# Kernel optimization log

Measured on AMD Instinct MI355X. Metric: run time of the kernel, lower is better.

## Reference

```python
import jax, jax.numpy as jnp
import numpy as np

B, Q, LE, D, P, A = 8, 32, 128, 512, 32, 128


def setup_inputs() -> dict:
    key = jax.random.key(0)
    ks = jax.random.split(key, 8)
    exp_tokens = jax.random.normal(ks[0], (B, Q, LE, D), dtype=jnp.float32)
    exp_mask = jax.random.randint(ks[1], (B, Q, LE), 0, 2, dtype=jnp.int32)
    s_j = jax.random.normal(ks[2], (B, P, D), dtype=jnp.float32)
    req_mask = jax.random.randint(ks[3], (B, P), 0, 2, dtype=jnp.int32)
    sc = 1.0 / np.sqrt(D)
    Ws_w = jax.random.normal(ks[4], (A, D), dtype=jnp.float32) * sc
    Ws_b = jax.random.normal(ks[5], (A,), dtype=jnp.float32) * 0.01
    U_w = jax.random.normal(ks[6], (A, D), dtype=jnp.float32) * sc
    v_w = jax.random.normal(ks[7], (1, A), dtype=jnp.float32) * (1.0 / np.sqrt(A))
    return {"exp_tokens": exp_tokens, "exp_mask": exp_mask, "s_j": s_j,
            "req_mask": req_mask, "Ws_w": Ws_w, "Ws_b": Ws_b, "U_w": U_w, "v_w": v_w}


def reference(exp_tokens, exp_mask, s_j, req_mask, Ws_w, Ws_b, U_w, v_w):
    # ws: (B,P,A); uh: (B,Q,Le,A)
    ws = jnp.einsum('bpd,ad->bpa', s_j, Ws_w) + Ws_b
    uh = jnp.einsum('bqtd,ad->bqta', exp_tokens, U_w)
    # broadcast add -> (B,Q,P,Le,A), tanh, project with v -> (B,Q,P,Le)
    scored = jnp.tanh(uh[:, :, None, :, :] + ws[:, None, :, None, :])
    e = jnp.einsum('bqpta,a->bqpt', scored, v_w[0])
    tok_mask = exp_mask[:, :, None, :]  # (B,Q,1,Le) broadcast over P
    e = jnp.where(tok_mask == 0, jnp.float32(-1e9), e)
    # joint softmax over Q*Le per (b,p)
    e_t = jnp.transpose(e, (0, 2, 1, 3)).reshape(e.shape[0], e.shape[2], -1)
    a = jax.nn.softmax(e_t, axis=-1).reshape(e.shape[0], e.shape[2], e.shape[1], e.shape[3])
    a = jnp.transpose(a, (0, 2, 1, 3))  # (B,Q,P,Le)
    s_rlk = jnp.einsum('bqpt,bqtd->bqpd', a, exp_tokens)
    rmask = req_mask[:, None, :, None].astype(s_rlk.dtype)
    return s_rlk * rmask
```

## Files before the change

kernel.cpp:

```cpp
#include <hip/hip_runtime.h>
#include <hip/hip_bf16.h>

#define B_  8
#define Q_  32
#define LE_ 128
#define D_  512
#define P_  32
#define A_  128

typedef __attribute__((ext_vector_type(8))) short short8_t;
typedef __attribute__((ext_vector_type(4))) float floatx4_t;

__device__ __forceinline__ short f2bf(float x) {
    unsigned u = __float_as_uint(x);
    unsigned r = (u + 0x7fffu + ((u >> 16) & 1u)) >> 16;
    return (short)r;
}

__global__ __launch_bounds__(128) void ws_kernel(
    const float* __restrict__ s_j, const float* __restrict__ Ws_w,
    const float* __restrict__ Ws_b, float* __restrict__ ws) {
    __shared__ float s_row[D_];
    int bp = blockIdx.x;
    const float* src = s_j + (size_t)bp * D_;
    for (int i = threadIdx.x; i < D_; i += 128) s_row[i] = src[i];
    __syncthreads();
    int a = threadIdx.x;
    const float4* w4 = (const float4*)(Ws_w + (size_t)a * D_);
    const float4* s4 = (const float4*)s_row;
    float acc = 0.0f;
#pragma unroll 8
    for (int i = 0; i < D_ / 4; ++i) {
        float4 w = w4[i];
        float4 s = s4[i];
        acc += w.x * s.x + w.y * s.y + w.z * s.z + w.w * s.w;
    }
    ws[bp * A_ + a] = __expf(2.0f * (acc + Ws_b[a]));
}

#define TM_ 64
#define TBK_ 64
#define LDSP_ 72

__global__ __launch_bounds__(256, 2) void uh_mfma_kernel(
    const float* __restrict__ X, const float* __restrict__ W,
    float* __restrict__ uh) {
    __shared__ short As[TM_ * LDSP_];
    __shared__ short Bs[A_ * LDSP_];
    int mblk = blockIdx.x * TM_;
    int tid = threadIdx.x;
    int wave = tid >> 6, lane = tid & 63;
    int qd = lane >> 4, lr = lane & 15;
    int mh = wave >> 1, nh = wave & 1;

    floatx4_t acc[2][4];
#pragma unroll
    for (int i = 0; i < 2; ++i)
#pragma unroll
        for (int j = 0; j < 4; ++j) acc[i][j] = (floatx4_t){0.f, 0.f, 0.f, 0.f};

    int ra = tid >> 2, qa = tid & 3;
    int rb = tid >> 1, hb = tid & 1;

    for (int kt = 0; kt < D_ / TBK_; ++kt) {
        int k0 = kt * TBK_;
        __syncthreads();
        {
            const float4* src = (const float4*)(X + (size_t)(mblk + ra) * D_ + k0 + qa * 16);
            short* dst = As + ra * LDSP_ + qa * 16;
#pragma unroll
            for (int j = 0; j < 2; ++j) {
                float4 v0 = src[j * 2 + 0];
                float4 v1 = src[j * 2 + 1];
                short8_t s;
                s[0] = f2bf(v0.x); s[1] = f2bf(v0.y); s[2] = f2bf(v0.z); s[3] = f2bf(v0.w);
                s[4] = f2bf(v1.x); s[5] = f2bf(v1.y); s[6] = f2bf(v1.z); s[7] = f2bf(v1.w);
                *(short8_t*)(dst + j * 8) = s;
            }
        }
        {
            const float4* src = (const float4*)(W + (size_t)rb * D_ + k0 + hb * 32);
            short* dst = Bs + rb * LDSP_ + hb * 32;
#pragma unroll
            for (int j = 0; j < 4; ++j) {
                float4 v0 = src[j * 2 + 0];
                float4 v1 = src[j * 2 + 1];
                short8_t s;
                s[0] = f2bf(v0.x); s[1] = f2bf(v0.y); s[2] = f2bf(v0.z); s[3] = f2bf(v0.w);
                s[4] = f2bf(v1.x); s[5] = f2bf(v1.y); s[6] = f2bf(v1.z); s[7] = f2bf(v1.w);
                *(short8_t*)(dst + j * 8) = s;
            }
        }
        __syncthreads();
#pragma unroll
        for (int ks = 0; ks < 2; ++ks) {
            short8_t af[2], bf[4];
#pragma unroll
            for (int i = 0; i < 2; ++i)
                af[i] = *(const short8_t*)(As + (mh * 32 + i * 16 + lr) * LDSP_ + ks * 32 + qd * 8);
#pragma unroll
            for (int j = 0; j < 4; ++j)
                bf[j] = *(const short8_t*)(Bs + (nh * 64 + j * 16 + lr) * LDSP_ + ks * 32 + qd * 8);
#pragma unroll
            for (int i = 0; i < 2; ++i)
#pragma unroll
                for (int j = 0; j < 4; ++j)
                    acc[i][j] = __builtin_amdgcn_mfma_f32_16x16x32_bf16(af[i], bf[j], acc[i][j], 0, 0, 0);
        }
    }
#pragma unroll
    for (int i = 0; i < 2; ++i) {
#pragma unroll
        for (int j = 0; j < 4; ++j) {
            int mg = mblk + mh * 32 + i * 16 + qd * 4;
            int ng = nh * 64 + j * 16 + lr;
            float* dst = uh + (size_t)mg * A_ + ng;
#pragma unroll
            for (int r = 0; r < 4; ++r)
                dst[(size_t)r * A_] = __expf(2.0f * acc[i][j][r]);
        }
    }
}

__global__ __launch_bounds__(256) void score_kernel(
    const float* __restrict__ EU, const float* __restrict__ EW,
    const float* __restrict__ v_w, const int* __restrict__ exp_mask,
    float* __restrict__ e) {
    __shared__ float eu_t[32][132];
    __shared__ float ew_t[32][128];
    __shared__ float n2v[128];
    int blk = blockIdx.x;
    int bq = blk >> 2, tc = blk & 3;
    int b = bq >> 5;
    int t0 = tc * 32;
    int tid = threadIdx.x;

#pragma unroll
    for (int i = 0; i < 4; ++i) {
        int f = tid + i * 256;
        int t = f >> 5, a4 = f & 31;
        float4 v = *(const float4*)(EU + (size_t)(bq * LE_ + t0 + t) * A_ + a4 * 4);
        *(float4*)&eu_t[t][a4 * 4] = v;
    }
#pragma unroll
    for (int i = 0; i < 4; ++i) {
        int f = tid + i * 256;
        int p = f >> 5, a4 = f & 31;
        *(float4*)&ew_t[p][a4 * 4] =
            *(const float4*)(EW + (size_t)(b * P_ + p) * A_ + a4 * 4);
    }
    if (tid < 32) {
        float4 v = *(const float4*)(v_w + tid * 4);
        v.x *= -2.0f; v.y *= -2.0f; v.z *= -2.0f; v.w *= -2.0f;
        *(float4*)&n2v[tid * 4] = v;
    }
    __syncthreads();

    float sumv = 0.0f;
#pragma unroll
    for (int i = 0; i < 32; ++i) {
        float4 nv = *(const float4*)&n2v[i * 4];
        sumv += nv.x + nv.y + nv.z + nv.w;
    }
    sumv *= -0.5f;

    int t = tid & 31, pb = tid >> 5;
    int mask = exp_mask[bq * LE_ + t0 + t];
    float acc[4] = {0.f, 0.f, 0.f, 0.f};
    for (int a4 = 0; a4 < 32; ++a4) {
        float4 u = *(const float4*)&eu_t[t][a4 * 4];
        float4 vv = *(const float4*)&n2v[a4 * 4];
#pragma unroll
        for (int i = 0; i < 4; ++i) {
            float4 w = *(const float4*)&ew_t[pb + i * 8][a4 * 4];
            acc[i] = fmaf(vv.x, __builtin_amdgcn_rcpf(1.0f + u.x * w.x), acc[i]);
            acc[i] = fmaf(vv.y, __builtin_amdgcn_rcpf(1.0f + u.y * w.y), acc[i]);
            acc[i] = fmaf(vv.z, __builtin_amdgcn_rcpf(1.0f + u.z * w.z), acc[i]);
            acc[i] = fmaf(vv.w, __builtin_amdgcn_rcpf(1.0f + u.w * w.w), acc[i]);
        }
    }
#pragma unroll
    for (int i = 0; i < 4; ++i) {
        int p = pb + i * 8;
        e[(size_t)(bq * P_ + p) * LE_ + t0 + t] = mask ? (sumv + acc[i]) : -1e9f;
    }
}

__global__ __launch_bounds__(256) void softmax_stats_kernel(
    const float* __restrict__ e, float* __restrict__ stats) {
    __shared__ float red[16];
    int bp = blockIdx.x;
    int b = bp >> 5, p = bp & 31;
    int tid = threadIdx.x;
    float vals[16];
#pragma unroll
    for (int i = 0; i < 16; ++i) {
        int idx = tid + i * 256;
        int q = idx >> 7, t = idx & 127;
        vals[i] = e[(size_t)((b * Q_ + q) * P_ + p) * LE_ + t];
    }
    float m = -1e30f;
#pragma unroll
    for (int i = 0; i < 16; ++i) m = fmaxf(m, vals[i]);
    for (int off = 32; off; off >>= 1) m = fmaxf(m, __shfl_down(m, off));
    int wid = tid >> 6;
    if ((tid & 63) == 0) red[wid] = m;
    __syncthreads();
    if (tid == 0)
        red[8] = fmaxf(fmaxf(red[0], red[1]), fmaxf(red[2], red[3]));
    __syncthreads();
    m = red[8];
    float s = 0.0f;
#pragma unroll
    for (int i = 0; i < 16; ++i) s += __expf(vals[i] - m);
    for (int off = 32; off; off >>= 1) s += __shfl_down(s, off);
    __syncthreads();
    if ((tid & 63) == 0) red[wid] = s;
    __syncthreads();
    if (tid == 0) {
        float ss = red[0] + red[1] + red[2] + red[3];
        stats[bp * 2 + 0] = m;
        stats[bp * 2 + 1] = 1.0f / ss;
    }
}

__global__ __launch_bounds__(256) void out_kernel(
    const float* __restrict__ e, const float* __restrict__ stats,
    const float* __restrict__ exp_tokens, const int* __restrict__ req_mask,
    float* __restrict__ out) {
    __shared__ float w_s[LE_ * P_];
    int bq = blockIdx.x >> 1, half = blockIdx.x & 1;
    int b = bq >> 5;
    int tid = threadIdx.x;

#pragma unroll
    for (int i = 0; i < 16; ++i) {
        int idx = tid + i * 256;
        int p = idx >> 7, t = idx & 127;
        int bp = b * P_ + p;
        float m = stats[bp * 2 + 0];
        float rm = req_mask[bp] ? stats[bp * 2 + 1] : 0.0f;
        float ev = e[(size_t)(bq * P_ + p) * LE_ + t];
        w_s[t * P_ + p] = __expf(ev - m) * rm;
    }
    __syncthreads();

    int d = half * 256 + tid;
    const float* T = exp_tokens + (size_t)bq * LE_ * D_;
    float acc[32];
#pragma unroll
    for (int p = 0; p < 32; ++p) acc[p] = 0.0f;

#pragma unroll 4
    for (int t = 0; t < LE_; ++t) {
        float tv = T[(size_t)t * D_ + d];
        const float4* wp = (const float4*)&w_s[t * P_];
#pragma unroll
        for (int j = 0; j < 8; ++j) {
            float4 w = wp[j];
            acc[j * 4 + 0] = fmaf(w.x, tv, acc[j * 4 + 0]);
            acc[j * 4 + 1] = fmaf(w.y, tv, acc[j * 4 + 1]);
            acc[j * 4 + 2] = fmaf(w.z, tv, acc[j * 4 + 2]);
            acc[j * 4 + 3] = fmaf(w.w, tv, acc[j * 4 + 3]);
        }
    }
    float* obase = out + (size_t)(bq * P_) * D_ + d;
#pragma unroll
    for (int p = 0; p < 32; ++p)
        obase[(size_t)p * D_] = acc[p];
}

extern "C" void kernel_launch(void* const* d_in, const int* in_sizes, int n_in,
                              void* d_out, int out_size, void* d_ws, size_t ws_size,
                              hipStream_t stream) {
    const float* exp_tokens = (const float*)d_in[0];
    const int*   exp_mask   = (const int*)d_in[1];
    const float* s_j        = (const float*)d_in[2];
    const int*   req_mask   = (const int*)d_in[3];
    const float* Ws_w       = (const float*)d_in[4];
    const float* Ws_b       = (const float*)d_in[5];
    const float* U_w        = (const float*)d_in[6];
    const float* v_w        = (const float*)d_in[7];
    float* out = (float*)d_out;

    float* ws_buf = (float*)d_ws;
    float* uh     = ws_buf + B_ * P_ * A_;
    float* e      = uh + (size_t)B_ * Q_ * LE_ * A_;
    float* stats  = e + (size_t)B_ * Q_ * P_ * LE_;

    ws_kernel<<<dim3(B_ * P_), dim3(128), 0, stream>>>(s_j, Ws_w, Ws_b, ws_buf);
    uh_mfma_kernel<<<dim3(B_ * Q_ * LE_ / TM_), dim3(256), 0, stream>>>(exp_tokens, U_w, uh);
    score_kernel<<<dim3(B_ * Q_ * 4), dim3(256), 0, stream>>>(uh, ws_buf, v_w, exp_mask, e);
    softmax_stats_kernel<<<dim3(B_ * P_), dim3(256), 0, stream>>>(e, stats);
    out_kernel<<<dim3(B_ * Q_ * 2), dim3(256), 0, stream>>>(e, stats, exp_tokens, req_mask, out);
}
```

Before: 194.7 us.

## Shrink uh GEMM tile, drop softmax max pass, split out_kernel by P halves

Several unrelated changes. The uh MFMA GEMM tile drops from 64 to 32 rows with four waves splitting N, and launch bounds rise to 4 blocks per CU for more blocks and occupancy. The score kernel folds 1+u*w into an fma. Softmax stats skips the max-subtraction pass and computes only 1/sum(exp(e)), relying on scores staying bounded (tanh output times v). This drops a reduction and a sync but risks overflow if scores were large. out_kernel now splits work by P halves instead of D halves, each thread handling two D columns with float2 loads and a padded LDS weight layout.

```diff
diff --git a/kernel.cpp b/kernel.cpp
--- a/kernel.cpp
+++ b/kernel.cpp
@@ -38,11 +38,11 @@
     ws[bp * A_ + a] = __expf(2.0f * (acc + Ws_b[a]));
 }
 
-#define TM_ 64
+#define TM_ 32
 #define TBK_ 64
 #define LDSP_ 72
 
-__global__ __launch_bounds__(256, 2) void uh_mfma_kernel(
+__global__ __launch_bounds__(256, 4) void uh_mfma_kernel(
     const float* __restrict__ X, const float* __restrict__ W,
     float* __restrict__ uh) {
     __shared__ short As[TM_ * LDSP_];
@@ -51,32 +51,28 @@
     int tid = threadIdx.x;
     int wave = tid >> 6, lane = tid & 63;
     int qd = lane >> 4, lr = lane & 15;
-    int mh = wave >> 1, nh = wave & 1;
-
-    floatx4_t acc[2][4];
+    int nq = wave;
+
+    floatx4_t acc[2][2];
 #pragma unroll
     for (int i = 0; i < 2; ++i)
 #pragma unroll
-        for (int j = 0; j < 4; ++j) acc[i][j] = (floatx4_t){0.f, 0.f, 0.f, 0.f};
-
-    int ra = tid >> 2, qa = tid & 3;
+        for (int j = 0; j < 2; ++j) acc[i][j] = (floatx4_t){0.f, 0.f, 0.f, 0.f};
+
+    int ra = tid >> 3, ea = tid & 7;
     int rb = tid >> 1, hb = tid & 1;
 
     for (int kt = 0; kt < D_ / TBK_; ++kt) {
         int k0 = kt * TBK_;
         __syncthreads();
         {
-            const float4* src = (const float4*)(X + (size_t)(mblk + ra) * D_ + k0 + qa * 16);
-            short* dst = As + ra * LDSP_ + qa * 16;
-#pragma unroll
-            for (int j = 0; j < 2; ++j) {
-                float4 v0 = src[j * 2 + 0];
-                float4 v1 = src[j * 2 + 1];
-                short8_t s;
-                s[0] = f2bf(v0.x); s[1] = f2bf(v0.y); s[2] = f2bf(v0.z); s[3] = f2bf(v0.w);
-                s[4] = f2bf(v1.x); s[5] = f2bf(v1.y); s[6] = f2bf(v1.z); s[7] = f2bf(v1.w);
-                *(short8_t*)(dst + j * 8) = s;
-            }
+            const float4* src = (const float4*)(X + (size_t)(mblk + ra) * D_ + k0 + ea * 8);
+            float4 v0 = src[0];
+            float4 v1 = src[1];
+            short8_t s;
+            s[0] = f2bf(v0.x); s[1] = f2bf(v0.y); s[2] = f2bf(v0.z); s[3] = f2bf(v0.w);
+            s[4] = f2bf(v1.x); s[5] = f2bf(v1.y); s[6] = f2bf(v1.z); s[7] = f2bf(v1.w);
+            *(short8_t*)(As + ra * LDSP_ + ea * 8) = s;
         }
         {
             const float4* src = (const float4*)(W + (size_t)rb * D_ + k0 + hb * 32);
@@ -94,26 +90,26 @@
         __syncthreads();
 #pragma unroll
         for (int ks = 0; ks < 2; ++ks) {
-            short8_t af[2], bf[4];
+            short8_t af[2], bfr[2];
 #pragma unroll
             for (int i = 0; i < 2; ++i)
-                af[i] = *(const short8_t*)(As + (mh * 32 + i * 16 + lr) * LDSP_ + ks * 32 + qd * 8);
-#pragma unroll
-            for (int j = 0; j < 4; ++j)
-                bf[j] = *(const short8_t*)(Bs + (nh * 64 + j * 16 + lr) * LDSP_ + ks * 32 + qd * 8);
+                af[i] = *(const short8_t*)(As + (i * 16 + lr) * LDSP_ + ks * 32 + qd * 8);
+#pragma unroll
+            for (int j = 0; j < 2; ++j)
+                bfr[j] = *(const short8_t*)(Bs + (nq * 32 + j * 16 + lr) * LDSP_ + ks * 32 + qd * 8);
 #pragma unroll
             for (int i = 0; i < 2; ++i)
 #pragma unroll
-                for (int j = 0; j < 4; ++j)
-                    acc[i][j] = __builtin_amdgcn_mfma_f32_16x16x32_bf16(af[i], bf[j], acc[i][j], 0, 0, 0);
+                for (int j = 0; j < 2; ++j)
+                    acc[i][j] = __builtin_amdgcn_mfma_f32_16x16x32_bf16(af[i], bfr[j], acc[i][j], 0, 0, 0);
         }
     }
 #pragma unroll
     for (int i = 0; i < 2; ++i) {
 #pragma unroll
-        for (int j = 0; j < 4; ++j) {
-            int mg = mblk + mh * 32 + i * 16 + qd * 4;
-            int ng = nh * 64 + j * 16 + lr;
+        for (int j = 0; j < 2; ++j) {
+            int mg = mblk + i * 16 + qd * 4;
+            int ng = nq * 32 + j * 16 + lr;
             float* dst = uh + (size_t)mg * A_ + ng;
 #pragma unroll
             for (int r = 0; r < 4; ++r)
@@ -173,10 +169,10 @@
 #pragma unroll
         for (int i = 0; i < 4; ++i) {
             float4 w = *(const float4*)&ew_t[pb + i * 8][a4 * 4];
-            acc[i] = fmaf(vv.x, __builtin_amdgcn_rcpf(1.0f + u.x * w.x), acc[i]);
-            acc[i] = fmaf(vv.y, __builtin_amdgcn_rcpf(1.0f + u.y * w.y), acc[i]);
-            acc[i] = fmaf(vv.z, __builtin_amdgcn_rcpf(1.0f + u.z * w.z), acc[i]);
-            acc[i] = fmaf(vv.w, __builtin_amdgcn_rcpf(1.0f + u.w * w.w), acc[i]);
+            acc[i] = fmaf(vv.x, __builtin_amdgcn_rcpf(fmaf(u.x, w.x, 1.0f)), acc[i]);
+            acc[i] = fmaf(vv.y, __builtin_amdgcn_rcpf(fmaf(u.y, w.y, 1.0f)), acc[i]);
+            acc[i] = fmaf(vv.z, __builtin_amdgcn_rcpf(fmaf(u.z, w.z, 1.0f)), acc[i]);
+            acc[i] = fmaf(vv.w, __builtin_amdgcn_rcpf(fmaf(u.w, w.w, 1.0f)), acc[i]);
         }
     }
 #pragma unroll
@@ -187,87 +183,75 @@
 }
 
 __global__ __launch_bounds__(256) void softmax_stats_kernel(
-    const float* __restrict__ e, float* __restrict__ stats) {
-    __shared__ float red[16];
+    const float* __restrict__ e, float* __restrict__ rinv) {
+    __shared__ float red[4];
     int bp = blockIdx.x;
     int b = bp >> 5, p = bp & 31;
     int tid = threadIdx.x;
-    float vals[16];
+    float s = 0.0f;
 #pragma unroll
     for (int i = 0; i < 16; ++i) {
         int idx = tid + i * 256;
         int q = idx >> 7, t = idx & 127;
-        vals[i] = e[(size_t)((b * Q_ + q) * P_ + p) * LE_ + t];
-    }
-    float m = -1e30f;
-#pragma unroll
-    for (int i = 0; i < 16; ++i) m = fmaxf(m, vals[i]);
-    for (int off = 32; off; off >>= 1) m = fmaxf(m, __shfl_down(m, off));
+        s += __expf(e[(size_t)((b * Q_ + q) * P_ + p) * LE_ + t]);
+    }
+    for (int off = 32; off; off >>= 1) s += __shfl_down(s, off);
     int wid = tid >> 6;
-    if ((tid & 63) == 0) red[wid] = m;
+    if ((tid & 63) == 0) red[wid] = s;
     __syncthreads();
     if (tid == 0)
-        red[8] = fmaxf(fmaxf(red[0], red[1]), fmaxf(red[2], red[3]));
-    __syncthreads();
-    m = red[8];
-    float s = 0.0f;
-#pragma unroll
-    for (int i = 0; i < 16; ++i) s += __expf(vals[i] - m);
-    for (int off = 32; off; off >>= 1) s += __shfl_down(s, off);
-    __syncthreads();
-    if ((tid & 63) == 0) red[wid] = s;
-    __syncthreads();
-    if (tid == 0) {
-        float ss = red[0] + red[1] + red[2] + red[3];
-        stats[bp * 2 + 0] = m;
-        stats[bp * 2 + 1] = 1.0f / ss;
-    }
-}
-
+        rinv[bp] = 1.0f / (red[0] + red[1] + red[2] + red[3]);
+}
+
+#define WSTRIDE 20
 __global__ __launch_bounds__(256) void out_kernel(
-    const float* __restrict__ e, const float* __restrict__ stats,
+    const float* __restrict__ e, const float* __restrict__ rinv,
     const float* __restrict__ exp_tokens, const int* __restrict__ req_mask,
     float* __restrict__ out) {
-    __shared__ float w_s[LE_ * P_];
-    int bq = blockIdx.x >> 1, half = blockIdx.x & 1;
+    __shared__ float w_s[LE_ * WSTRIDE];
+    int bq = blockIdx.x >> 1, ph = blockIdx.x & 1;
     int b = bq >> 5;
-    int tid = threadIdx.x;
-
-#pragma unroll
-    for (int i = 0; i < 16; ++i) {
+    int p0 = ph * 16;
+    int tid = threadIdx.x;
+
+#pragma unroll
+    for (int i = 0; i < 8; ++i) {
         int idx = tid + i * 256;
-        int p = idx >> 7, t = idx & 127;
-        int bp = b * P_ + p;
-        float m = stats[bp * 2 + 0];
-        float rm = req_mask[bp] ? stats[bp * 2 + 1] : 0.0f;
-        float ev = e[(size_t)(bq * P_ + p) * LE_ + t];
-        w_s[t * P_ + p] = __expf(ev - m) * rm;
-    }
-    __syncthreads();
-
-    int d = half * 256 + tid;
+        int t = idx & 127, p = idx >> 7;
+        int bp = b * P_ + p0 + p;
+        float rm = req_mask[bp] ? rinv[bp] : 0.0f;
+        float ev = e[(size_t)(bq * P_ + p0 + p) * LE_ + t];
+        w_s[t * WSTRIDE + p] = __expf(ev) * rm;
+    }
+    __syncthreads();
+
+    int d0 = tid * 2;
     const float* T = exp_tokens + (size_t)bq * LE_ * D_;
-    float acc[32];
-#pragma unroll
-    for (int p = 0; p < 32; ++p) acc[p] = 0.0f;
+    float2 acc2[16];
+#pragma unroll
+    for (int p = 0; p < 16; ++p) acc2[p] = make_float2(0.f, 0.f);
 
 #pragma unroll 4
     for (int t = 0; t < LE_; ++t) {
-        float tv = T[(size_t)t * D_ + d];
-        const float4* wp = (const float4*)&w_s[t * P_];
-#pragma unroll
-        for (int j = 0; j < 8; ++j) {
+        float2 tv = *(const float2*)&T[(size_t)t * D_ + d0];
+        const float4* wp = (const float4*)&w_s[t * WSTRIDE];
+#pragma unroll
+        for (int j = 0; j < 4; ++j) {
             float4 w = wp[j];
-            acc[j * 4 + 0] = fmaf(w.x, tv, acc[j * 4 + 0]);
-            acc[j * 4 + 1] = fmaf(w.y, tv, acc[j * 4 + 1]);
-            acc[j * 4 + 2] = fmaf(w.z, tv, acc[j * 4 + 2]);
-            acc[j * 4 + 3] = fmaf(w.w, tv, acc[j * 4 + 3]);
-        }
-    }
-    float* obase = out + (size_t)(bq * P_) * D_ + d;
-#pragma unroll
-    for (int p = 0; p < 32; ++p)
-        obase[(size_t)p * D_] = acc[p];
+            acc2[j * 4 + 0].x = fmaf(w.x, tv.x, acc2[j * 4 + 0].x);
+            acc2[j * 4 + 0].y = fmaf(w.x, tv.y, acc2[j * 4 + 0].y);
+            acc2[j * 4 + 1].x = fmaf(w.y, tv.x, acc2[j * 4 + 1].x);
+            acc2[j * 4 + 1].y = fmaf(w.y, tv.y, acc2[j * 4 + 1].y);
+            acc2[j * 4 + 2].x = fmaf(w.z, tv.x, acc2[j * 4 + 2].x);
+            acc2[j * 4 + 2].y = fmaf(w.z, tv.y, acc2[j * 4 + 2].y);
+            acc2[j * 4 + 3].x = fmaf(w.w, tv.x, acc2[j * 4 + 3].x);
+            acc2[j * 4 + 3].y = fmaf(w.w, tv.y, acc2[j * 4 + 3].y);
+        }
+    }
+    float* obase = out + (size_t)(bq * P_ + p0) * D_ + d0;
+#pragma unroll
+    for (int p = 0; p < 16; ++p)
+        *(float2*)(obase + (size_t)p * D_) = acc2[p];
 }
 
 extern "C" void kernel_launch(void* const* d_in, const int* in_sizes, int n_in,
@@ -286,11 +270,11 @@
     float* ws_buf = (float*)d_ws;
     float* uh     = ws_buf + B_ * P_ * A_;
     float* e      = uh + (size_t)B_ * Q_ * LE_ * A_;
-    float* stats  = e + (size_t)B_ * Q_ * P_ * LE_;
+    float* rinv   = e + (size_t)B_ * Q_ * P_ * LE_;
 
     ws_kernel<<<dim3(B_ * P_), dim3(128), 0, stream>>>(s_j, Ws_w, Ws_b, ws_buf);
     uh_mfma_kernel<<<dim3(B_ * Q_ * LE_ / TM_), dim3(256), 0, stream>>>(exp_tokens, U_w, uh);
     score_kernel<<<dim3(B_ * Q_ * 4), dim3(256), 0, stream>>>(uh, ws_buf, v_w, exp_mask, e);
-    softmax_stats_kernel<<<dim3(B_ * P_), dim3(256), 0, stream>>>(e, stats);
-    out_kernel<<<dim3(B_ * Q_ * 2), dim3(256), 0, stream>>>(e, stats, exp_tokens, req_mask, out);
-}
+    softmax_stats_kernel<<<dim3(B_ * P_), dim3(256), 0, stream>>>(e, rinv);
+    out_kernel<<<dim3(B_ * Q_ * 2), dim3(256), 0, stream>>>(e, rinv, exp_tokens, req_mask, out);
+}
```

Result: slower. 202.7 us (+4.1%).
